# Optimization experiments

Measured on AMD Instinct MI355X. Metric: run time of the kernel, lower is better.

The kernel has to match this reference:

```python
import math
import jax, jax.numpy as jnp
import numpy as np

N_HEAD = 16
LORA_SCALE = 16.0 / 8.0  # lora_alpha / r


def lora_linear(x, W, b, A, B):
    # y = x @ W^T + b + scale * (x @ A^T) @ B^T
    base = jnp.einsum('btc,oc->bto', x, W) + b
    low = jnp.einsum('btc,rc->btr', x, A)
    return base + LORA_SCALE * jnp.einsum('btr,or->bto', low, B)


def setup_inputs() -> dict:
    key = jax.random.key(0)
    ks = jax.random.split(key, 8)
    B, T, C = 2, 2048, 1024
    r = 8
    s = 0.02
    return {
        'x': jax.random.normal(ks[0], (B, T, C), jnp.float32),
        'W_attn': jax.random.normal(ks[1], (3 * C, C), jnp.float32) * s,
        'b_attn': jnp.zeros((3 * C,), jnp.float32),
        'A_attn': jax.random.normal(ks[2], (r, C), jnp.float32) * s,
        'B_attn': jax.random.normal(ks[3], (3 * C, r), jnp.float32) * s,
        'W_proj': jax.random.normal(ks[4], (C, C), jnp.float32) * s,
        'b_proj': jnp.zeros((C,), jnp.float32),
        'A_proj': jax.random.normal(ks[5], (r, C), jnp.float32) * s,
        'B_proj': jax.random.normal(ks[6], (C, r), jnp.float32) * s,
    }


def reference(x, W_attn, b_attn, A_attn, B_attn, W_proj, b_proj, A_proj, B_proj):
    B, T, C = x.shape
    H = N_HEAD
    hd = C // H
    qkv = lora_linear(x, W_attn, b_attn, A_attn, B_attn)  # [B,T,3C]
    q, k, v = jnp.split(qkv, 3, axis=2)
    # [B,H,T,hd]
    q = q.reshape(B, T, H, hd).transpose(0, 2, 1, 3)
    k = k.reshape(B, T, H, hd).transpose(0, 2, 1, 3)
    v = v.reshape(B, T, H, hd).transpose(0, 2, 1, 3)
    att = jnp.einsum('bhqd,bhkd->bhqk', q, k) * (1.0 / math.sqrt(hd))
    causal = jnp.tril(jnp.ones((T, T), bool))
    att = jnp.where(causal, att, -jnp.inf)
    att = jax.nn.softmax(att, axis=-1)
    out = jnp.einsum('bhqk,bhkd->bhqd', att, v)
    out = out.transpose(0, 2, 1, 3).reshape(B, T, C)
    return lora_linear(out, W_proj, b_proj, A_proj, B_proj)
```

## Files before the change

### kernel.cpp

```cpp
#include <hip/hip_runtime.h>
#include <hip/hip_bf16.h>
#include <stdint.h>

typedef __bf16 bf16_t;
typedef __bf16 bf16x8 __attribute__((ext_vector_type(8)));
typedef __bf16 bf16x4 __attribute__((ext_vector_type(4)));
typedef __bf16 bf16x2 __attribute__((ext_vector_type(2)));
typedef float f32x4 __attribute__((ext_vector_type(4)));
typedef float f32x16 __attribute__((ext_vector_type(16)));
typedef uint32_t u32;
typedef uint32_t u32x4 __attribute__((ext_vector_type(4)));

typedef __attribute__((address_space(1))) void as1void;
typedef __attribute__((address_space(3))) void as3void;

#define QSCALE 0.18033688011112042f

__constant__ unsigned char kOrder[24] = {7, 20, 22, 23, 6, 16, 18, 19, 21,
                                         5, 12, 14, 15, 17, 4, 8, 10, 11, 13,
                                         3, 9, 2, 1, 0};

__device__ __forceinline__ void gll16(const void* g, void* l) {
  __builtin_amdgcn_global_load_lds((as1void*)g, (as3void*)l, 16, 0, 0);
}

__device__ __forceinline__ u32 pack2(float a, float b) {
  bf16x2 t = {(bf16_t)a, (bf16_t)b};
  return __builtin_bit_cast(u32, t);
}

__global__ void prep_all(const float* __restrict__ W_attn, const float* __restrict__ B_attn,
                         const float* __restrict__ A_attn, const float* __restrict__ W_proj,
                         const float* __restrict__ B_proj, const float* __restrict__ A_proj,
                         const float4* __restrict__ x,
                         bf16_t* __restrict__ WaE, bf16_t* __restrict__ WpE,
                         bf16x4* __restrict__ Xb) {
  int bid = blockIdx.x;
  if (bid < 16384) {
    int idx = bid * 256 + threadIdx.x;
    const float *W, *Bm, *Am;
    bf16_t* dst;
    if (idx < 3145728) {
      W = W_attn; Bm = B_attn; Am = A_attn; dst = WaE;
    } else {
      idx -= 3145728;
      W = W_proj; Bm = B_proj; Am = A_proj; dst = WpE;
    }
    int o = idx >> 10, c = idx & 1023;
    float acc = W[idx];
#pragma unroll
    for (int r = 0; r < 8; ++r)
      acc += 2.0f * Bm[o * 8 + r] * Am[r * 1024 + c];
    dst[idx] = (bf16_t)acc;
  } else {
    int i = (bid - 16384) * 256 + threadIdx.x;
    float4 v = x[i];
    bf16x4 o = {(bf16_t)v.x, (bf16_t)v.y, (bf16_t)v.z, (bf16_t)v.w};
    Xb[i] = o;
  }
}

__global__ __launch_bounds__(256) void transpose_v(
    const bf16_t* __restrict__ Vb, bf16_t* __restrict__ Vtg) {
  __shared__ bf16_t Lt[128][72];
  int blk = blockIdx.x;
  int bh = blk >> 4, tb = blk & 15;
  int t0 = tb * 128;
  int tid = threadIdx.x;
  {
    int t = tid >> 1, dc = (tid & 1) * 32;
    const bf16_t* p = Vb + (size_t)bh * 131072 + (size_t)(t0 + t) * 64 + dc;
#pragma unroll
    for (int u = 0; u < 4; ++u)
      *(bf16x8*)&Lt[t][dc + u * 8] = *(const bf16x8*)(p + u * 8);
  }
  __syncthreads();
  int d = tid & 63, tg = tid >> 6;
  bf16_t* q = Vtg + (size_t)bh * 131072 + (size_t)d * 2048 + t0 + tg * 32;
#pragma unroll
  for (int u = 0; u < 4; ++u) {
    bf16x8 v;
#pragma unroll
    for (int e = 0; e < 8; ++e) v[e] = Lt[tg * 32 + u * 8 + e][d];
    *(bf16x8*)(q + u * 8) = v;
  }
}

template <bool QKV>
__global__ __launch_bounds__(256, 3) void gemm_bt(
    const bf16_t* __restrict__ A, const bf16_t* __restrict__ Bt,
    const float* __restrict__ bias,
    bf16_t* __restrict__ Qb, bf16_t* __restrict__ Kb, bf16_t* __restrict__ Vb,
    float* __restrict__ Out) {
  __shared__ bf16_t Als[128][64];
  __shared__ bf16_t Bls[128][64];
  int mb, nb;
  if (QKV) {
    int id = blockIdx.x;
    int xcd = id & 7, s = id >> 3;
    int half = s >= 48 ? 1 : 0;
    int within = s - 48 * half;
    int cm = within & 7, cn = within >> 3;
    int chunkIdx = half * 8 + xcd;
    mb = (chunkIdx & 3) * 8 + cm;
    nb = (chunkIdx >> 2) * 6 + cn;
  } else {
    int id = blockIdx.x;
    int xcd = id & 7, s = id >> 3;
    mb = (xcd & 3) * 8 + (s & 7);
    nb = (xcd >> 2) * 4 + (s >> 3);
  }
  const int m0 = mb * 128;
  const int n0 = nb * 128;
  const int tid = threadIdx.x;
  const int lane = tid & 63;
  const int w = tid >> 6;
  const int wm = w >> 1, wn = w & 1;
  const int lr = lane & 15, g = lane >> 4;
  const int sw = (lane & 7) << 3;
  const int srow = lane >> 3;
  const int soff = ((lane & 7) ^ srow) * 8;

  f32x4 acc[4][4] = {};

  for (int k0 = 0; k0 < 1024; k0 += 64) {
#pragma unroll
    for (int c = 0; c < 4; ++c) {
      int r = w * 32 + c * 8 + srow;
      gll16(A + (size_t)(m0 + r) * 1024 + k0 + soff, &Als[w * 32 + c * 8][0]);
      gll16(Bt + (size_t)(n0 + r) * 1024 + k0 + soff, &Bls[w * 32 + c * 8][0]);
    }
    __syncthreads();
#pragma unroll
    for (int ks = 0; ks < 2; ++ks) {
      bf16x8 af[4], bfv[4];
#pragma unroll
      for (int i = 0; i < 4; ++i)
        af[i] = *(const bf16x8*)&Als[wm * 64 + i * 16 + lr][(ks * 32 + g * 8) ^ sw];
#pragma unroll
      for (int j = 0; j < 4; ++j)
        bfv[j] = *(const bf16x8*)&Bls[wn * 64 + j * 16 + lr][(ks * 32 + g * 8) ^ sw];
#pragma unroll
      for (int i = 0; i < 4; ++i)
#pragma unroll
        for (int j = 0; j < 4; ++j)
          acc[i][j] = __builtin_amdgcn_mfma_f32_16x16x32_bf16(af[i], bfv[j], acc[i][j], 0, 0, 0);
    }
    __syncthreads();
  }

#pragma unroll
  for (int i = 0; i < 4; ++i) {
#pragma unroll
    for (int j = 0; j < 4; ++j) {
#pragma unroll
      for (int e = 0; e < 4; ++e) {
        int m = m0 + wm * 64 + i * 16 + g * 4 + e;
        int n = n0 + wn * 64 + j * 16 + lr;
        float v = acc[i][j][e] + bias[n];
        if (QKV) {
          int b = m >> 11, t = m & 2047;
          int which = n >> 10, hn = n & 1023;
          int h = hn >> 6, d = hn & 63;
          if (which == 0) v *= QSCALE;
          bf16_t* dst = (which == 0) ? Qb : (which == 1) ? Kb : Vb;
          dst[(((size_t)(b * 16 + h)) * 2048 + t) * 64 + d] = (bf16_t)v;
        } else {
          Out[(size_t)m * 1024 + n] = v;
        }
      }
    }
  }
}

__global__ __launch_bounds__(256, 2) void attn_fwd(
    const bf16_t* __restrict__ Qb, const bf16_t* __restrict__ Kb,
    const bf16_t* __restrict__ Vtg, bf16_t* __restrict__ Ob,
    bf16_t* __restrict__ Po, float* __restrict__ Pml) {
  __shared__ bf16_t Kls[2][128][64];
  __shared__ bf16_t Vt[2][64][128];

  int id = blockIdx.x;
  int xcd = id & 7, r = id >> 3;
  int bh = xcd * 4 + (r & 3);
  int j = kOrder[r >> 2];
  int qb, kt0, kt1, part;
  if (j < 8) {
    qb = j; kt0 = 0; kt1 = qb + 1; part = -1;
  } else {
    qb = 8 + ((j - 8) >> 1);
    part = (j - 8) & 1;
    int kts = qb + 1, nA = (kts + 1) >> 1;
    kt0 = part ? nA : 0;
    kt1 = part ? kts : nA;
  }
  int b = bh >> 4, h = bh & 15;

  const int tid = threadIdx.x, lane = tid & 63, w = tid >> 6;
  const int q32 = lane & 31;
  const int hi = lane >> 5;
  const int ksw = (q32 & 7) << 3;
  const int vkey = ((q32 & 7) ^ (q32 >> 2)) << 3;
  const bf16_t* Qp = Qb + (size_t)bh * 2048 * 64;
  const bf16_t* Kp = Kb + (size_t)bh * 2048 * 64;
  const bf16_t* Vtp = Vtg + (size_t)bh * 131072;

  const int q0 = qb * 128;
  const int qrow = q0 + w * 32 + q32;

  const int ksr = lane >> 3;
  const int kso = ((lane & 7) ^ ksr) * 8;
  int vdo[4];
#pragma unroll
  for (int cc = 0; cc < 4; ++cc) {
    int d = 16 * w + 4 * cc + (lane >> 4);
    int key = (d & 7) ^ ((d >> 2) & 7);
    vdo[cc] = d * 2048 + (((lane & 15) ^ key) << 3);
  }

  bf16x8 qf[4];
#pragma unroll
  for (int ds = 0; ds < 4; ++ds)
    qf[ds] = *(const bf16x8*)(Qp + (size_t)qrow * 64 + ds * 16 + hi * 8);

  float m_run = -3e38f, l_run = 0.f;
  f32x16 o_acc[2] = {};

  {
    const int kp = kt0 * 128;
#pragma unroll
    for (int c = 0; c < 4; ++c) {
      int rb = w * 32 + c * 8;
      gll16(Kp + (size_t)(kp + rb + ksr) * 64 + kso, &Kls[0][rb][0]);
    }
#pragma unroll
    for (int cc = 0; cc < 4; ++cc)
      gll16(Vtp + vdo[cc] + kp, &Vt[0][16 * w + 4 * cc][0]);
    __syncthreads();
  }

  int cb = 0;
  for (int kt = kt0; kt < kt1; ++kt) {
    const bool haveNext = (kt + 1 < kt1);
    const bool maskt = (kt == qb);
    const int nfa = maskt ? (w + 1) : 4;
    const int nb = cb ^ 1;

    if (haveNext) {
      const int kn = (kt + 1) * 128;
#pragma unroll
      for (int c = 0; c < 4; ++c) {
        int rb = w * 32 + c * 8;
        gll16(Kp + (size_t)(kn + rb + ksr) * 64 + kso, &Kls[nb][rb][0]);
      }
#pragma unroll
      for (int cc = 0; cc < 4; ++cc)
        gll16(Vtp + vdo[cc] + kn, &Vt[nb][16 * w + 4 * cc][0]);
    }

    f32x16 s[4] = {};
    __builtin_amdgcn_s_setprio(1);
#pragma unroll
    for (int fa = 0; fa < 4; ++fa) {
      if (fa < nfa) {
#pragma unroll
        for (int ds = 0; ds < 4; ++ds) {
          bf16x8 kf = *(const bf16x8*)&Kls[cb][fa * 32 + q32][(ds * 16 + hi * 8) ^ ksw];
          s[fa] = __builtin_amdgcn_mfma_f32_32x32x16_bf16(kf, qf[ds], s[fa], 0, 0, 0);
        }
      }
    }
    __builtin_amdgcn_s_setprio(0);

    float mloc = -3e38f;
#pragma unroll
    for (int fa = 0; fa < 4; ++fa) {
      if (fa < nfa) {
        if (maskt && fa == w) {
#pragma unroll
          for (int rr = 0; rr < 16; ++rr) {
            int km = (rr & 3) + 8 * (rr >> 2) + 4 * hi;
            if (km > q32) s[fa][rr] = -3e38f;
          }
        }
#pragma unroll
        for (int rr = 0; rr < 16; ++rr) mloc = fmaxf(mloc, s[fa][rr]);
      }
    }
    mloc = fmaxf(mloc, __shfl_xor(mloc, 32, 64));
    if (!__all(mloc <= m_run + 8.0f)) {
      float mnew = fmaxf(m_run, mloc);
      float rs = __builtin_amdgcn_exp2f(m_run - mnew);
      m_run = mnew;
      l_run *= rs;
      o_acc[0] *= rs;
      o_acc[1] *= rs;
    }

    float lsum = 0.f;
#pragma unroll
    for (int fa = 0; fa < 4; ++fa) {
      if (fa < nfa) {
        float p[16];
#pragma unroll
        for (int rr = 0; rr < 16; ++rr) {
          p[rr] = __builtin_amdgcn_exp2f(s[fa][rr] - m_run);
          lsum += p[rr];
        }
        u32 x0 = pack2(p[0], p[1]),   x1 = pack2(p[2], p[3]);
        u32 x2 = pack2(p[4], p[5]),   x3 = pack2(p[6], p[7]);
        u32 y0 = pack2(p[8], p[9]),   y1 = pack2(p[10], p[11]);
        u32 y2 = pack2(p[12], p[13]), y3 = pack2(p[14], p[15]);
        u32 z0 = hi ? x0 : x2;
        u32 z1 = hi ? x1 : x3;
        u32 z2 = hi ? y0 : y2;
        u32 z3 = hi ? y1 : y3;
        z0 = (u32)__shfl_xor((int)z0, 32, 64);
        z1 = (u32)__shfl_xor((int)z1, 32, 64);
        z2 = (u32)__shfl_xor((int)z2, 32, 64);
        z3 = (u32)__shfl_xor((int)z3, 32, 64);
        u32x4 pw0 = hi ? (u32x4){z0, z1, x2, x3} : (u32x4){x0, x1, z0, z1};
        u32x4 pw1 = hi ? (u32x4){z2, z3, y2, y3} : (u32x4){y0, y1, z2, z3};
        bf16x8 P0 = __builtin_bit_cast(bf16x8, pw0);
        bf16x8 P1 = __builtin_bit_cast(bf16x8, pw1);
        __builtin_amdgcn_s_setprio(1);
#pragma unroll
        for (int db = 0; db < 2; ++db) {
          int d = db * 32 + q32;
          bf16x8 vf0 = *(const bf16x8*)&Vt[cb][d][(fa * 32 + hi * 8) ^ vkey];
          o_acc[db] = __builtin_amdgcn_mfma_f32_32x32x16_bf16(vf0, P0, o_acc[db], 0, 0, 0);
          bf16x8 vf1 = *(const bf16x8*)&Vt[cb][d][(fa * 32 + 16 + hi * 8) ^ vkey];
          o_acc[db] = __builtin_amdgcn_mfma_f32_32x32x16_bf16(vf1, P1, o_acc[db], 0, 0, 0);
        }
        __builtin_amdgcn_s_setprio(0);
      }
    }
    lsum += __shfl_xor(lsum, 32, 64);
    l_run += lsum;

    __syncthreads();
    cb = nb;
  }

  const int prow = w * 32 + q32;
  if (part < 0) {
    float inv = 1.0f / l_run;
    bf16_t* obase = Ob + ((size_t)(b * 2048 + qrow)) * 1024 + h * 64;
#pragma unroll
    for (int db = 0; db < 2; ++db) {
#pragma unroll
      for (int rg = 0; rg < 4; ++rg) {
        bf16x4 ov = {(bf16_t)(o_acc[db][rg * 4 + 0] * inv),
                     (bf16_t)(o_acc[db][rg * 4 + 1] * inv),
                     (bf16_t)(o_acc[db][rg * 4 + 2] * inv),
                     (bf16_t)(o_acc[db][rg * 4 + 3] * inv)};
        *(bf16x4*)(obase + db * 32 + rg * 8 + hi * 4) = ov;
      }
    }
  } else {
    int sidx = bh * 16 + (qb - 8) * 2 + part;
    bf16_t* po = (part == 0)
        ? Ob + ((size_t)(b * 2048 + qrow)) * 1024 + h * 64
        : Po + (size_t)(bh * 8 + (qb - 8)) * 8192 + prow * 64;
    int stride = (part == 0) ? 1 : 1;
    (void)stride;
#pragma unroll
    for (int db = 0; db < 2; ++db) {
#pragma unroll
      for (int rg = 0; rg < 4; ++rg) {
        bf16x4 ov = {(bf16_t)o_acc[db][rg * 4 + 0], (bf16_t)o_acc[db][rg * 4 + 1],
                     (bf16_t)o_acc[db][rg * 4 + 2], (bf16_t)o_acc[db][rg * 4 + 3]};
        *(bf16x4*)(po + db * 32 + rg * 8 + hi * 4) = ov;
      }
    }
    if (hi == 0) {
      Pml[sidx * 256 + prow * 2] = m_run;
      Pml[sidx * 256 + prow * 2 + 1] = l_run;
    }
  }
}

__global__ __launch_bounds__(256) void attn_merge(
    const bf16_t* __restrict__ Po, const float* __restrict__ Pml,
    bf16_t* __restrict__ Ob) {
  int blk = blockIdx.x;
  int bh = blk >> 3, qb8 = blk & 7;
  int qb = 8 + qb8;
  int b = bh >> 4, h = bh & 15;
  int sA = bh * 16 + qb8 * 2, sB = sA + 1;
  int t = threadIdx.x;
  int row = t >> 1, c0 = (t & 1) * 32;

  float mA = Pml[sA * 256 + row * 2], lA = Pml[sA * 256 + row * 2 + 1];
  float mB = Pml[sB * 256 + row * 2], lB = Pml[sB * 256 + row * 2 + 1];
  float m = fmaxf(mA, mB);
  float wA = __builtin_amdgcn_exp2f(mA - m);
  float wB = __builtin_amdgcn_exp2f(mB - m);
  float inv = 1.0f / (lA * wA + lB * wB);
  wA *= inv;
  wB *= inv;

  bf16_t* ob = Ob + ((size_t)(b * 2048 + qb * 128 + row)) * 1024 + h * 64 + c0;
  const bf16_t* pb = Po + (size_t)(bh * 8 + qb8) * 8192 + row * 64 + c0;
#pragma unroll
  for (int u = 0; u < 4; ++u) {
    bf16x8 a = *(const bf16x8*)(ob + u * 8);
    bf16x8 c = *(const bf16x8*)(pb + u * 8);
    bf16x8 o;
#pragma unroll
    for (int i = 0; i < 8; ++i)
      o[i] = (bf16_t)((float)a[i] * wA + (float)c[i] * wB);
    *(bf16x8*)(ob + u * 8) = o;
  }
}

extern "C" void kernel_launch(void* const* d_in, const int* in_sizes, int n_in,
                              void* d_out, int out_size, void* d_ws, size_t ws_size,
                              hipStream_t stream) {
  const float* x      = (const float*)d_in[0];
  const float* W_attn = (const float*)d_in[1];
  const float* b_attn = (const float*)d_in[2];
  const float* A_attn = (const float*)d_in[3];
  const float* B_attn = (const float*)d_in[4];
  const float* W_proj = (const float*)d_in[5];
  const float* b_proj = (const float*)d_in[6];
  const float* A_proj = (const float*)d_in[7];
  const float* B_proj = (const float*)d_in[8];
  float* out = (float*)d_out;

  char* ws = (char*)d_ws;
  bf16_t* WaE = (bf16_t*)(ws);
  bf16_t* WpE = (bf16_t*)(ws + 6291456);
  bf16_t* Xb  = (bf16_t*)(ws + 8388608);
  bf16_t* Qb  = (bf16_t*)(ws + 16777216);
  bf16_t* Kb  = (bf16_t*)(ws + 25165824);
  bf16_t* Vb  = (bf16_t*)(ws + 33554432);
  bf16_t* Ob  = (bf16_t*)(ws + 41943040);
  bf16_t* Vtg = (bf16_t*)(ws + 8388608);
  bf16_t* Po  = (bf16_t*)(ws);
  float*  Pml = (float*)(ws + 4194304);

  prep_all<<<20480, 256, 0, stream>>>(W_attn, B_attn, A_attn, W_proj, B_proj, A_proj,
                                      (const float4*)x, WaE, WpE, (bf16x4*)Xb);

  gemm_bt<true><<<768, 256, 0, stream>>>(Xb, WaE, b_attn, Qb, Kb, Vb, nullptr);
  transpose_v<<<512, 256, 0, stream>>>(Vb, Vtg);
  attn_fwd<<<768, 256, 0, stream>>>(Qb, Kb, Vtg, Ob, Po, Pml);
  attn_merge<<<256, 256, 0, stream>>>(Po, Pml, Ob);
  gemm_bt<false><<<256, 256, 0, stream>>>(Ob, WpE, b_proj, nullptr, nullptr, nullptr, out);
}
```

Measured before the change: 119.5 us.

## Halve attention KV tile to 64 keys, raise occupancy, drop GEMM XCD swizzle

The attention kernel now streams 64-key K/V tiles instead of 128, which halves its shared memory and raises the launch-bounds occupancy hint from 2 to 4 blocks per CU. Causal masking is reworked per wave so waves fully above the diagonal skip the tile, and the V swizzle is simplified to match K. The block schedule order is also reshuffled, and the GEMMs drop their XCD-aware block remapping in favour of a plain 2D grid. The smaller tiles mean more loop iterations and barriers, and removing the XCD mapping may hurt L2 locality in the GEMMs.

```diff
diff --git a/kernel.cpp b/kernel.cpp
--- a/kernel.cpp
+++ b/kernel.cpp
@@ -16,9 +16,9 @@
 
 #define QSCALE 0.18033688011112042f
 
-__constant__ unsigned char kOrder[24] = {7, 20, 22, 23, 6, 16, 18, 19, 21,
-                                         5, 12, 14, 15, 17, 4, 8, 10, 11, 13,
-                                         3, 9, 2, 1, 0};
+__constant__ unsigned char kOrder[24] = {7, 22, 23, 20, 21, 6, 18, 19, 16, 17,
+                                         5, 14, 15, 12, 13, 4, 10, 11, 8, 9,
+                                         3, 2, 1, 0};
 
 __device__ __forceinline__ void gll16(const void* g, void* l) {
   __builtin_amdgcn_global_load_lds((as1void*)g, (as3void*)l, 16, 0, 0);
@@ -94,24 +94,8 @@
     float* __restrict__ Out) {
   __shared__ bf16_t Als[128][64];
   __shared__ bf16_t Bls[128][64];
-  int mb, nb;
-  if (QKV) {
-    int id = blockIdx.x;
-    int xcd = id & 7, s = id >> 3;
-    int half = s >= 48 ? 1 : 0;
-    int within = s - 48 * half;
-    int cm = within & 7, cn = within >> 3;
-    int chunkIdx = half * 8 + xcd;
-    mb = (chunkIdx & 3) * 8 + cm;
-    nb = (chunkIdx >> 2) * 6 + cn;
-  } else {
-    int id = blockIdx.x;
-    int xcd = id & 7, s = id >> 3;
-    mb = (xcd & 3) * 8 + (s & 7);
-    nb = (xcd >> 2) * 4 + (s >> 3);
-  }
-  const int m0 = mb * 128;
-  const int n0 = nb * 128;
+  const int m0 = blockIdx.x * 128;
+  const int n0 = blockIdx.y * 128;
   const int tid = threadIdx.x;
   const int lane = tid & 63;
   const int w = tid >> 6;
@@ -173,12 +157,12 @@
   }
 }
 
-__global__ __launch_bounds__(256, 2) void attn_fwd(
+__global__ __launch_bounds__(256, 4) void attn_fwd(
     const bf16_t* __restrict__ Qb, const bf16_t* __restrict__ Kb,
     const bf16_t* __restrict__ Vtg, bf16_t* __restrict__ Ob,
     bf16_t* __restrict__ Po, float* __restrict__ Pml) {
-  __shared__ bf16_t Kls[2][128][64];
-  __shared__ bf16_t Vt[2][64][128];
+  __shared__ bf16_t Kls[2][64][64];
+  __shared__ bf16_t Vt[2][64][64];
 
   int id = blockIdx.x;
   int xcd = id & 7, r = id >> 3;
@@ -186,13 +170,13 @@
   int j = kOrder[r >> 2];
   int qb, kt0, kt1, part;
   if (j < 8) {
-    qb = j; kt0 = 0; kt1 = qb + 1; part = -1;
+    qb = j; kt0 = 0; kt1 = 2 * qb + 2; part = -1;
   } else {
     qb = 8 + ((j - 8) >> 1);
     part = (j - 8) & 1;
-    int kts = qb + 1, nA = (kts + 1) >> 1;
+    int nA = qb + 1;
     kt0 = part ? nA : 0;
-    kt1 = part ? kts : nA;
+    kt1 = part ? (2 * qb + 2) : nA;
   }
   int b = bh >> 4, h = bh & 15;
 
@@ -200,7 +184,6 @@
   const int q32 = lane & 31;
   const int hi = lane >> 5;
   const int ksw = (q32 & 7) << 3;
-  const int vkey = ((q32 & 7) ^ (q32 >> 2)) << 3;
   const bf16_t* Qp = Qb + (size_t)bh * 2048 * 64;
   const bf16_t* Kp = Kb + (size_t)bh * 2048 * 64;
   const bf16_t* Vtp = Vtg + (size_t)bh * 131072;
@@ -208,15 +191,12 @@
   const int q0 = qb * 128;
   const int qrow = q0 + w * 32 + q32;
 
-  const int ksr = lane >> 3;
-  const int kso = ((lane & 7) ^ ksr) * 8;
-  int vdo[4];
-#pragma unroll
-  for (int cc = 0; cc < 4; ++cc) {
-    int d = 16 * w + 4 * cc + (lane >> 4);
-    int key = (d & 7) ^ ((d >> 2) & 7);
-    vdo[cc] = d * 2048 + (((lane & 15) ^ key) << 3);
-  }
+  const int sr = lane >> 3;
+  const int sc = ((lane & 7) ^ sr) * 8;
+  int vdo[2];
+#pragma unroll
+  for (int c = 0; c < 2; ++c)
+    vdo[c] = (w * 16 + c * 8 + sr) * 2048 + sc;
 
   bf16x8 qf[4];
 #pragma unroll
@@ -227,116 +207,124 @@
   f32x16 o_acc[2] = {};
 
   {
-    const int kp = kt0 * 128;
-#pragma unroll
-    for (int c = 0; c < 4; ++c) {
-      int rb = w * 32 + c * 8;
-      gll16(Kp + (size_t)(kp + rb + ksr) * 64 + kso, &Kls[0][rb][0]);
-    }
-#pragma unroll
-    for (int cc = 0; cc < 4; ++cc)
-      gll16(Vtp + vdo[cc] + kp, &Vt[0][16 * w + 4 * cc][0]);
+    const int kp = kt0 * 64;
+#pragma unroll
+    for (int c = 0; c < 2; ++c) {
+      int rb = w * 16 + c * 8;
+      gll16(Kp + (size_t)(kp + rb + sr) * 64 + sc, &Kls[0][rb][0]);
+      gll16(Vtp + vdo[c] + kp, &Vt[0][rb][0]);
+    }
     __syncthreads();
   }
 
   int cb = 0;
   for (int kt = kt0; kt < kt1; ++kt) {
     const bool haveNext = (kt + 1 < kt1);
-    const bool maskt = (kt == qb);
-    const int nfa = maskt ? (w + 1) : 4;
     const int nb = cb ^ 1;
 
     if (haveNext) {
-      const int kn = (kt + 1) * 128;
-#pragma unroll
-      for (int c = 0; c < 4; ++c) {
-        int rb = w * 32 + c * 8;
-        gll16(Kp + (size_t)(kn + rb + ksr) * 64 + kso, &Kls[nb][rb][0]);
-      }
-#pragma unroll
-      for (int cc = 0; cc < 4; ++cc)
-        gll16(Vtp + vdo[cc] + kn, &Vt[nb][16 * w + 4 * cc][0]);
-    }
-
-    f32x16 s[4] = {};
-    __builtin_amdgcn_s_setprio(1);
-#pragma unroll
-    for (int fa = 0; fa < 4; ++fa) {
-      if (fa < nfa) {
-#pragma unroll
-        for (int ds = 0; ds < 4; ++ds) {
-          bf16x8 kf = *(const bf16x8*)&Kls[cb][fa * 32 + q32][(ds * 16 + hi * 8) ^ ksw];
-          s[fa] = __builtin_amdgcn_mfma_f32_32x32x16_bf16(kf, qf[ds], s[fa], 0, 0, 0);
-        }
-      }
-    }
-    __builtin_amdgcn_s_setprio(0);
-
-    float mloc = -3e38f;
-#pragma unroll
-    for (int fa = 0; fa < 4; ++fa) {
-      if (fa < nfa) {
-        if (maskt && fa == w) {
-#pragma unroll
-          for (int rr = 0; rr < 16; ++rr) {
-            int km = (rr & 3) + 8 * (rr >> 2) + 4 * hi;
-            if (km > q32) s[fa][rr] = -3e38f;
+      const int kn = (kt + 1) * 64;
+#pragma unroll
+      for (int c = 0; c < 2; ++c) {
+        int rb = w * 16 + c * 8;
+        gll16(Kp + (size_t)(kn + rb + sr) * 64 + sc, &Kls[nb][rb][0]);
+        gll16(Vtp + vdo[c] + kn, &Vt[nb][rb][0]);
+      }
+    }
+
+    const int rel = kt - 2 * qb;
+    int nfa = 2, dfa = -1;
+    if (rel == 0) {
+      if (w == 0) { nfa = 1; dfa = 0; }
+      else if (w == 1) { dfa = 1; }
+    } else if (rel == 1) {
+      if (w < 2) nfa = 0;
+      else if (w == 2) { nfa = 1; dfa = 0; }
+      else { dfa = 1; }
+    }
+
+    if (nfa > 0) {
+      f32x16 s[2] = {};
+      __builtin_amdgcn_s_setprio(1);
+#pragma unroll
+      for (int fa = 0; fa < 2; ++fa) {
+        if (fa < nfa) {
+#pragma unroll
+          for (int ds = 0; ds < 4; ++ds) {
+            bf16x8 kf = *(const bf16x8*)&Kls[cb][fa * 32 + q32][(ds * 16 + hi * 8) ^ ksw];
+            s[fa] = __builtin_amdgcn_mfma_f32_32x32x16_bf16(kf, qf[ds], s[fa], 0, 0, 0);
           }
         }
-#pragma unroll
-        for (int rr = 0; rr < 16; ++rr) mloc = fmaxf(mloc, s[fa][rr]);
-      }
-    }
-    mloc = fmaxf(mloc, __shfl_xor(mloc, 32, 64));
-    if (!__all(mloc <= m_run + 8.0f)) {
-      float mnew = fmaxf(m_run, mloc);
-      float rs = __builtin_amdgcn_exp2f(m_run - mnew);
-      m_run = mnew;
-      l_run *= rs;
-      o_acc[0] *= rs;
-      o_acc[1] *= rs;
-    }
-
-    float lsum = 0.f;
-#pragma unroll
-    for (int fa = 0; fa < 4; ++fa) {
-      if (fa < nfa) {
-        float p[16];
-#pragma unroll
-        for (int rr = 0; rr < 16; ++rr) {
-          p[rr] = __builtin_amdgcn_exp2f(s[fa][rr] - m_run);
-          lsum += p[rr];
+      }
+      __builtin_amdgcn_s_setprio(0);
+
+      float mloc = -3e38f;
+#pragma unroll
+      for (int fa = 0; fa < 2; ++fa) {
+        if (fa < nfa) {
+          if (fa == dfa) {
+#pragma unroll
+            for (int rr = 0; rr < 16; ++rr) {
+              int km = (rr & 3) + 8 * (rr >> 2) + 4 * hi;
+              if (km > q32) s[fa][rr] = -3e38f;
+            }
+          }
+#pragma unroll
+          for (int rr = 0; rr < 16; rr += 2)
+            mloc = fmaxf(mloc, fmaxf(s[fa][rr], s[fa][rr + 1]));
         }
-        u32 x0 = pack2(p[0], p[1]),   x1 = pack2(p[2], p[3]);
-        u32 x2 = pack2(p[4], p[5]),   x3 = pack2(p[6], p[7]);
-        u32 y0 = pack2(p[8], p[9]),   y1 = pack2(p[10], p[11]);
-        u32 y2 = pack2(p[12], p[13]), y3 = pack2(p[14], p[15]);
-        u32 z0 = hi ? x0 : x2;
-        u32 z1 = hi ? x1 : x3;
-        u32 z2 = hi ? y0 : y2;
-        u32 z3 = hi ? y1 : y3;
-        z0 = (u32)__shfl_xor((int)z0, 32, 64);
-        z1 = (u32)__shfl_xor((int)z1, 32, 64);
-        z2 = (u32)__shfl_xor((int)z2, 32, 64);
-        z3 = (u32)__shfl_xor((int)z3, 32, 64);
-        u32x4 pw0 = hi ? (u32x4){z0, z1, x2, x3} : (u32x4){x0, x1, z0, z1};
-        u32x4 pw1 = hi ? (u32x4){z2, z3, y2, y3} : (u32x4){y0, y1, z2, z3};
-        bf16x8 P0 = __builtin_bit_cast(bf16x8, pw0);
-        bf16x8 P1 = __builtin_bit_cast(bf16x8, pw1);
-        __builtin_amdgcn_s_setprio(1);
-#pragma unroll
-        for (int db = 0; db < 2; ++db) {
-          int d = db * 32 + q32;
-          bf16x8 vf0 = *(const bf16x8*)&Vt[cb][d][(fa * 32 + hi * 8) ^ vkey];
-          o_acc[db] = __builtin_amdgcn_mfma_f32_32x32x16_bf16(vf0, P0, o_acc[db], 0, 0, 0);
-          bf16x8 vf1 = *(const bf16x8*)&Vt[cb][d][(fa * 32 + 16 + hi * 8) ^ vkey];
-          o_acc[db] = __builtin_amdgcn_mfma_f32_32x32x16_bf16(vf1, P1, o_acc[db], 0, 0, 0);
+      }
+      mloc = fmaxf(mloc, __shfl_xor(mloc, 32, 64));
+      if (!__all(mloc <= m_run + 8.0f)) {
+        float mnew = fmaxf(m_run, mloc);
+        float rs = __builtin_amdgcn_exp2f(m_run - mnew);
+        m_run = mnew;
+        l_run *= rs;
+        o_acc[0] *= rs;
+        o_acc[1] *= rs;
+      }
+
+      float lsum = 0.f;
+#pragma unroll
+      for (int fa = 0; fa < 2; ++fa) {
+        if (fa < nfa) {
+          float p[16];
+#pragma unroll
+          for (int rr = 0; rr < 16; ++rr) {
+            p[rr] = __builtin_amdgcn_exp2f(s[fa][rr] - m_run);
+            lsum += p[rr];
+          }
+          u32 x0 = pack2(p[0], p[1]),   x1 = pack2(p[2], p[3]);
+          u32 x2 = pack2(p[4], p[5]),   x3 = pack2(p[6], p[7]);
+          u32 y0 = pack2(p[8], p[9]),   y1 = pack2(p[10], p[11]);
+          u32 y2 = pack2(p[12], p[13]), y3 = pack2(p[14], p[15]);
+          u32 z0 = hi ? x0 : x2;
+          u32 z1 = hi ? x1 : x3;
+          u32 z2 = hi ? y0 : y2;
+          u32 z3 = hi ? y1 : y3;
+          z0 = (u32)__shfl_xor((int)z0, 32, 64);
+          z1 = (u32)__shfl_xor((int)z1, 32, 64);
+          z2 = (u32)__shfl_xor((int)z2, 32, 64);
+          z3 = (u32)__shfl_xor((int)z3, 32, 64);
+          u32x4 pw0 = hi ? (u32x4){z0, z1, x2, x3} : (u32x4){x0, x1, z0, z1};
+          u32x4 pw1 = hi ? (u32x4){z2, z3, y2, y3} : (u32x4){y0, y1, z2, z3};
+          bf16x8 P0 = __builtin_bit_cast(bf16x8, pw0);
+          bf16x8 P1 = __builtin_bit_cast(bf16x8, pw1);
+          __builtin_amdgcn_s_setprio(1);
+#pragma unroll
+          for (int db = 0; db < 2; ++db) {
+            int d = db * 32 + q32;
+            bf16x8 vf0 = *(const bf16x8*)&Vt[cb][d][(fa * 32 + hi * 8) ^ ksw];
+            o_acc[db] = __builtin_amdgcn_mfma_f32_32x32x16_bf16(vf0, P0, o_acc[db], 0, 0, 0);
+            bf16x8 vf1 = *(const bf16x8*)&Vt[cb][d][(fa * 32 + 16 + hi * 8) ^ ksw];
+            o_acc[db] = __builtin_amdgcn_mfma_f32_32x32x16_bf16(vf1, P1, o_acc[db], 0, 0, 0);
+          }
+          __builtin_amdgcn_s_setprio(0);
         }
-        __builtin_amdgcn_s_setprio(0);
-      }
-    }
-    lsum += __shfl_xor(lsum, 32, 64);
-    l_run += lsum;
+      }
+      lsum += __shfl_xor(lsum, 32, 64);
+      l_run += lsum;
+    }
 
     __syncthreads();
     cb = nb;
@@ -362,8 +350,6 @@
     bf16_t* po = (part == 0)
         ? Ob + ((size_t)(b * 2048 + qrow)) * 1024 + h * 64
         : Po + (size_t)(bh * 8 + (qb - 8)) * 8192 + prow * 64;
-    int stride = (part == 0) ? 1 : 1;
-    (void)stride;
 #pragma unroll
     for (int db = 0; db < 2; ++db) {
 #pragma unroll
@@ -443,9 +429,9 @@
   prep_all<<<20480, 256, 0, stream>>>(W_attn, B_attn, A_attn, W_proj, B_proj, A_proj,
                                       (const float4*)x, WaE, WpE, (bf16x4*)Xb);
 
-  gemm_bt<true><<<768, 256, 0, stream>>>(Xb, WaE, b_attn, Qb, Kb, Vb, nullptr);
+  gemm_bt<true><<<dim3(32, 24), 256, 0, stream>>>(Xb, WaE, b_attn, Qb, Kb, Vb, nullptr);
   transpose_v<<<512, 256, 0, stream>>>(Vb, Vtg);
   attn_fwd<<<768, 256, 0, stream>>>(Qb, Kb, Vtg, Ob, Po, Pml);
   attn_merge<<<256, 256, 0, stream>>>(Po, Pml, Ob);
-  gemm_bt<false><<<256, 256, 0, stream>>>(Ob, WpE, b_proj, nullptr, nullptr, nullptr, out);
-}
+  gemm_bt<false><<<dim3(32, 8), 256, 0, stream>>>(Ob, WpE, b_proj, nullptr, nullptr, nullptr, out);
+}
```

Measured after the change: 116.3 us. 2.6% less time.
